# Kernel optimization log

Hardware: AMD Instinct MI355X
Metric: run time of the kernel (lower is better)

Reference implementation:

```python
import jax, jax.numpy as jnp
import numpy as np


def setup_inputs() -> dict:
    key = jax.random.key(0)
    kx, ky = jax.random.split(key)
    n, m, d = 2048, 2048, 16  # d == n_wires
    x = jax.random.normal(kx, (n, d), dtype=jnp.float32)
    y = jax.random.normal(ky, (m, d), dtype=jnp.float32)
    return {"x": x, "y": y}


def reference(x, y):
    # RY gates on distinct wires commute; RY(-y_k) RY(x_k) = RY(x_k - y_k).
    # State = tensor product over wires of RY(x_k - y_k)|0>, so the |0...0>
    # amplitude is prod_k cos((x_k - y_k)/2). Original code stores abs(amplitude).
    half_diff = 0.5 * (x[:, None, :] - y[None, :, :])  # [n, m, d]
    kernel = jnp.abs(jnp.prod(jnp.cos(half_diff), axis=-1))  # [n, m]
    return kernel
```

## Files before the change

kernel.cpp:

```cpp
#include <hip/hip_runtime.h>
#include <hip/hip_bf16.h>


constexpr int D = 16;

typedef short  bf16x8 __attribute__((ext_vector_type(8)));
typedef float  f32x4  __attribute__((ext_vector_type(4)));

static __device__ inline unsigned int pk2(float a, float b) {
    __hip_bfloat16 ha = __float2bfloat16(a);
    __hip_bfloat16 hb = __float2bfloat16(b);
    unsigned short ua, ub;
    __builtin_memcpy(&ua, &ha, 2);
    __builtin_memcpy(&ub, &hb, 2);
    return (unsigned int)ua | ((unsigned int)ub << 16);
}

__global__ __launch_bounds__(256)
void precs(const float* __restrict__ x, const float* __restrict__ y,
           unsigned short* __restrict__ Arow, unsigned short* __restrict__ Bcol,
           int n, int ntot) {
    const int u = blockIdx.x * 256 + threadIdx.x;
    if (u >= ntot) return;
    const bool isrow = (u < n);
    const float* src = isrow ? (x + (size_t)u * D) : (y + (size_t)(u - n) * D);
    unsigned short* dst =
        isrow ? (Arow + (size_t)u * 64) : (Bcol + (size_t)(u - n) * 64);
    const float scale = isrow ? 0.5f : 1.0f;

    float f[8][4];
#pragma unroll
    for (int p = 0; p < 8; ++p) {
        const float a0 = src[2 * p], a1 = src[2 * p + 1];
        float sm, cm, sp, cp;
        __sincosf(0.5f * (a0 - a1), &sm, &cm);
        __sincosf(0.5f * (a0 + a1), &sp, &cp);
        f[p][0] = scale * cm; f[p][1] = scale * sm;
        f[p][2] = scale * cp; f[p][3] = scale * sp;
    }
#pragma unroll
    for (int q = 0; q < 4; ++q) {
        uint4 lo, hi;
        lo.x = pk2(f[2*q][0]*f[2*q+1][0], f[2*q][0]*f[2*q+1][1]);
        lo.y = pk2(f[2*q][0]*f[2*q+1][2], f[2*q][0]*f[2*q+1][3]);
        lo.z = pk2(f[2*q][1]*f[2*q+1][0], f[2*q][1]*f[2*q+1][1]);
        lo.w = pk2(f[2*q][1]*f[2*q+1][2], f[2*q][1]*f[2*q+1][3]);
        hi.x = pk2(f[2*q][2]*f[2*q+1][0], f[2*q][2]*f[2*q+1][1]);
        hi.y = pk2(f[2*q][2]*f[2*q+1][2], f[2*q][2]*f[2*q+1][3]);
        hi.z = pk2(f[2*q][3]*f[2*q+1][0], f[2*q][3]*f[2*q+1][1]);
        hi.w = pk2(f[2*q][3]*f[2*q+1][2], f[2*q][3]*f[2*q+1][3]);
        *(uint4*)(dst + q * 16)     = lo;
        *(uint4*)(dst + q * 16 + 8) = hi;
    }
}

__global__ __launch_bounds__(256)
void qkern(const unsigned short* __restrict__ Arow,
           const unsigned short* __restrict__ Bcol,
           float* __restrict__ out, int m) {
    const int tid  = threadIdx.x;
    const int wave = tid >> 6;
    const int lane = tid & 63;
    const int m16  = lane & 15;
    const int half = lane >> 4;
    const int row0 = blockIdx.x * 64 + wave * 16;
    const int col0 = blockIdx.y * 64;

    const bf16x8 zf = {0, 0, 0, 0, 0, 0, 0, 0};
    const f32x4  zc = {0.f, 0.f, 0.f, 0.f};

    bf16x8 af[4];
#pragma unroll
    for (int q = 0; q < 4; ++q)
        af[q] = (half < 2)
            ? *(const bf16x8*)(Arow + (size_t)(row0 + m16) * 64 + q * 16 + half * 8)
            : zf;

#pragma unroll
    for (int cg = 0; cg < 4; ++cg) {
        const int colb = col0 + cg * 16;
        f32x4 acc[4];
#pragma unroll
        for (int q = 0; q < 4; ++q) {
            const bf16x8 bfq = (half < 2)
                ? *(const bf16x8*)(Bcol + (size_t)(colb + m16) * 64 + q * 16 + half * 8)
                : zf;
            acc[q] = __builtin_amdgcn_mfma_f32_16x16x32_bf16(af[q], bfq, zc, 0, 0, 0);
        }
#pragma unroll
        for (int r = 0; r < 4; ++r) {
            const float v =
                fabsf(acc[0][r] * acc[1][r] * acc[2][r] * acc[3][r]);
            const int row = row0 + half * 4 + r;
            __builtin_nontemporal_store(v, out + (size_t)row * m + colb + m16);
        }
    }
}

extern "C" void kernel_launch(void* const* d_in, const int* in_sizes, int n_in,
                              void* d_out, int out_size, void* d_ws, size_t ws_size,
                              hipStream_t stream) {
    const float* x = (const float*)d_in[0];
    const float* y = (const float*)d_in[1];
    float* out = (float*)d_out;
    const int n = in_sizes[0] / D;
    const int m = in_sizes[1] / D;

    unsigned short* Arow = (unsigned short*)d_ws;
    unsigned short* Bcol = Arow + (size_t)n * 64;

    const int ntot = n + m;
    precs<<<(ntot + 255) / 256, 256, 0, stream>>>(x, y, Arow, Bcol, n, ntot);

    dim3 grid(n / 64, m / 64);
    qkern<<<grid, 256, 0, stream>>>(Arow, Bcol, out, m);
}
```

Measured before the change: 68.78 us.

## Fuse trig feature precompute into MFMA kernel via shared memory

```diff
diff --git a/kernel.cpp b/kernel.cpp
--- a/kernel.cpp
+++ b/kernel.cpp
@@ -3,6 +3,7 @@
 
 
 constexpr int D = 16;
+constexpr int RSTR = 72;
 
 typedef short  bf16x8 __attribute__((ext_vector_type(8)));
 typedef float  f32x4  __attribute__((ext_vector_type(4)));
@@ -17,54 +18,61 @@
 }
 
 __global__ __launch_bounds__(256)
-void precs(const float* __restrict__ x, const float* __restrict__ y,
-           unsigned short* __restrict__ Arow, unsigned short* __restrict__ Bcol,
-           int n, int ntot) {
-    const int u = blockIdx.x * 256 + threadIdx.x;
-    if (u >= ntot) return;
-    const bool isrow = (u < n);
-    const float* src = isrow ? (x + (size_t)u * D) : (y + (size_t)(u - n) * D);
-    unsigned short* dst =
-        isrow ? (Arow + (size_t)u * 64) : (Bcol + (size_t)(u - n) * 64);
-    const float scale = isrow ? 0.5f : 1.0f;
+void qkern(const float* __restrict__ x, const float* __restrict__ y,
+           float* __restrict__ out, int m) {
+    __shared__ unsigned short Al[64 * RSTR];
+    __shared__ unsigned short Bl[64 * RSTR];
 
-    float f[8][4];
+    const int tid  = threadIdx.x;
+    const int row0b = blockIdx.x * 64;
+    const int col0b = blockIdx.y * 64;
+
+    {
+        const int u    = tid >> 1;
+        const int half = tid & 1;
+        const bool isrow = (u < 64);
+        const float* src = isrow ? (x + (size_t)(row0b + u) * D)
+                                 : (y + (size_t)(col0b + (u - 64)) * D);
+        unsigned short* dst = (isrow ? Al + (size_t)u * RSTR
+                                     : Bl + (size_t)(u - 64) * RSTR);
+        const float scale = isrow ? 0.5f : 1.0f;
+
+        float f[4][4];
 #pragma unroll
-    for (int p = 0; p < 8; ++p) {
-        const float a0 = src[2 * p], a1 = src[2 * p + 1];
-        float sm, cm, sp, cp;
-        __sincosf(0.5f * (a0 - a1), &sm, &cm);
-        __sincosf(0.5f * (a0 + a1), &sp, &cp);
-        f[p][0] = scale * cm; f[p][1] = scale * sm;
-        f[p][2] = scale * cp; f[p][3] = scale * sp;
+        for (int pp = 0; pp < 4; ++pp) {
+            const int p = half * 4 + pp;
+            const float a0 = src[2 * p], a1 = src[2 * p + 1];
+            float sm, cm, sp, cp;
+            __sincosf(0.5f * (a0 - a1), &sm, &cm);
+            __sincosf(0.5f * (a0 + a1), &sp, &cp);
+            f[pp][0] = scale * cm; f[pp][1] = scale * sm;
+            f[pp][2] = scale * cp; f[pp][3] = scale * sp;
+        }
+#pragma unroll
+        for (int qq = 0; qq < 2; ++qq) {
+            const int q = half * 2 + qq;
+            const float* fa = f[2 * qq];
+            const float* fb = f[2 * qq + 1];
+            uint4 lo, hi;
+            lo.x = pk2(fa[0] * fb[0], fa[0] * fb[1]);
+            lo.y = pk2(fa[0] * fb[2], fa[0] * fb[3]);
+            lo.z = pk2(fa[1] * fb[0], fa[1] * fb[1]);
+            lo.w = pk2(fa[1] * fb[2], fa[1] * fb[3]);
+            hi.x = pk2(fa[2] * fb[0], fa[2] * fb[1]);
+            hi.y = pk2(fa[2] * fb[2], fa[2] * fb[3]);
+            hi.z = pk2(fa[3] * fb[0], fa[3] * fb[1]);
+            hi.w = pk2(fa[3] * fb[2], fa[3] * fb[3]);
+            *(uint4*)(dst + q * 16)     = lo;
+            *(uint4*)(dst + q * 16 + 8) = hi;
+        }
     }
-#pragma unroll
-    for (int q = 0; q < 4; ++q) {
-        uint4 lo, hi;
-        lo.x = pk2(f[2*q][0]*f[2*q+1][0], f[2*q][0]*f[2*q+1][1]);
-        lo.y = pk2(f[2*q][0]*f[2*q+1][2], f[2*q][0]*f[2*q+1][3]);
-        lo.z = pk2(f[2*q][1]*f[2*q+1][0], f[2*q][1]*f[2*q+1][1]);
-        lo.w = pk2(f[2*q][1]*f[2*q+1][2], f[2*q][1]*f[2*q+1][3]);
-        hi.x = pk2(f[2*q][2]*f[2*q+1][0], f[2*q][2]*f[2*q+1][1]);
-        hi.y = pk2(f[2*q][2]*f[2*q+1][2], f[2*q][2]*f[2*q+1][3]);
-        hi.z = pk2(f[2*q][3]*f[2*q+1][0], f[2*q][3]*f[2*q+1][1]);
-        hi.w = pk2(f[2*q][3]*f[2*q+1][2], f[2*q][3]*f[2*q+1][3]);
-        *(uint4*)(dst + q * 16)     = lo;
-        *(uint4*)(dst + q * 16 + 8) = hi;
-    }
-}
+    __syncthreads();
 
-__global__ __launch_bounds__(256)
-void qkern(const unsigned short* __restrict__ Arow,
-           const unsigned short* __restrict__ Bcol,
-           float* __restrict__ out, int m) {
-    const int tid  = threadIdx.x;
     const int wave = tid >> 6;
     const int lane = tid & 63;
     const int m16  = lane & 15;
-    const int half = lane >> 4;
-    const int row0 = blockIdx.x * 64 + wave * 16;
-    const int col0 = blockIdx.y * 64;
+    const int kh   = lane >> 4;
+    const int rw0  = wave * 16;
 
     const bf16x8 zf = {0, 0, 0, 0, 0, 0, 0, 0};
     const f32x4  zc = {0.f, 0.f, 0.f, 0.f};
@@ -72,27 +80,25 @@
     bf16x8 af[4];
 #pragma unroll
     for (int q = 0; q < 4; ++q)
-        af[q] = (half < 2)
-            ? *(const bf16x8*)(Arow + (size_t)(row0 + m16) * 64 + q * 16 + half * 8)
+        af[q] = (kh < 2)
+            ? *(const bf16x8*)(Al + (size_t)(rw0 + m16) * RSTR + q * 16 + kh * 8)
             : zf;
 
 #pragma unroll
     for (int cg = 0; cg < 4; ++cg) {
-        const int colb = col0 + cg * 16;
         f32x4 acc[4];
 #pragma unroll
         for (int q = 0; q < 4; ++q) {
-            const bf16x8 bfq = (half < 2)
-                ? *(const bf16x8*)(Bcol + (size_t)(colb + m16) * 64 + q * 16 + half * 8)
+            const bf16x8 bfq = (kh < 2)
+                ? *(const bf16x8*)(Bl + (size_t)(cg * 16 + m16) * RSTR + q * 16 + kh * 8)
                 : zf;
             acc[q] = __builtin_amdgcn_mfma_f32_16x16x32_bf16(af[q], bfq, zc, 0, 0, 0);
         }
 #pragma unroll
         for (int r = 0; r < 4; ++r) {
-            const float v =
-                fabsf(acc[0][r] * acc[1][r] * acc[2][r] * acc[3][r]);
-            const int row = row0 + half * 4 + r;
-            __builtin_nontemporal_store(v, out + (size_t)row * m + colb + m16);
+            const float v = fabsf(acc[0][r] * acc[1][r] * acc[2][r] * acc[3][r]);
+            const int row = row0b + rw0 + kh * 4 + r;
+            __builtin_nontemporal_store(v, out + (size_t)row * m + col0b + cg * 16 + m16);
         }
     }
 }
@@ -106,12 +112,6 @@
     const int n = in_sizes[0] / D;
     const int m = in_sizes[1] / D;
 
-    unsigned short* Arow = (unsigned short*)d_ws;
-    unsigned short* Bcol = Arow + (size_t)n * 64;
-
-    const int ntot = n + m;
-    precs<<<(ntot + 255) / 256, 256, 0, stream>>>(x, y, Arow, Bcol, n, ntot);
-
     dim3 grid(n / 64, m / 64);
-    qkern<<<grid, 256, 0, stream>>>(Arow, Bcol, out, m);
+    qkern<<<grid, 256, 0, stream>>>(x, y, out, m);
 }
```

New measurement: 62.22 us. 1.11x faster.
